# Kernel optimization log

Hardware: AMD Instinct MI355X
Metric: run time of the kernel (lower is better)

## Reference

```python
import jax, jax.numpy as jnp
import numpy as np

N_NODES = 50000
N_EDGES = 800000
IN_FEAT = 4
HIDDEN = 128
NUM_LAYERS = 3


def setup_inputs() -> dict:
    key = jax.random.key(0)
    ks = jax.random.split(key, 16)
    x = jax.random.normal(ks[0], (N_NODES, IN_FEAT), dtype=jnp.float32)
    edge_index = jax.random.randint(ks[1], (2, N_EDGES), 0, N_NODES, dtype=jnp.int64)

    def lin(k, fan_in, fan_out):
        bound = 1.0 / np.sqrt(fan_in)
        k1, k2 = jax.random.split(k)
        W = jax.random.uniform(k1, (fan_in, fan_out), minval=-bound, maxval=bound, dtype=jnp.float32)
        b = jax.random.uniform(k2, (fan_out,), minval=-bound, maxval=bound, dtype=jnp.float32)
        return W, b

    W_enc, b_enc = lin(ks[2], IN_FEAT, HIDDEN)
    W_g1, b_g1 = lin(ks[3], HIDDEN, HIDDEN)
    W_g2, b_g2 = lin(ks[4], HIDDEN, HIDDEN)
    W_g3, b_g3 = lin(ks[5], HIDDEN, HIDDEN)
    W_m1, b_m1 = lin(ks[6], 2 * HIDDEN, HIDDEN)
    W_m2, b_m2 = lin(ks[7], HIDDEN, 3)
    return {
        "x": x, "edge_index": edge_index,
        "W_enc": W_enc, "b_enc": b_enc,
        "W_g1": W_g1, "b_g1": b_g1,
        "W_g2": W_g2, "b_g2": b_g2,
        "W_g3": W_g3, "b_g3": b_g3,
        "W_m1": W_m1, "b_m1": b_m1,
        "W_m2": W_m2, "b_m2": b_m2,
    }


def _gcn_forward(x, edge_index, W_enc, b_enc, gcn_params, W_m1, b_m1, W_m2, b_m2):
    n = x.shape[0]
    # Node encoder (linear + ReLU) -> [N, H]
    h = jax.nn.relu(x @ W_enc + b_enc)

    # Add self-loops once (GCNConv default add_self_loops=True)
    src = jnp.concatenate([edge_index[0], jnp.arange(n, dtype=edge_index.dtype)])
    dst = jnp.concatenate([edge_index[1], jnp.arange(n, dtype=edge_index.dtype)])
    # Symmetric degree normalization: D^{-1/2} (A+I) D^{-1/2}
    deg = jax.ops.segment_sum(jnp.ones_like(dst, dtype=h.dtype), dst, num_segments=n)
    deg_inv_sqrt = jnp.where(deg > 0, jax.lax.rsqrt(jnp.maximum(deg, 1.0)), 0.0)
    norm = (deg_inv_sqrt[src] * deg_inv_sqrt[dst])[:, None]  # [E+N, 1]

    for (W, b) in gcn_params:
        m = (h @ W)[src] * norm                       # gather + scale messages
        h = jax.ops.segment_sum(m, dst, num_segments=n) + b
        h = jax.nn.relu(h)                            # dropout is identity at eval

    # Edge classifier: gather endpoints, concat, MLP -> [E, 3]
    ef = jnp.concatenate([h[edge_index[0]], h[edge_index[1]]], axis=-1)
    return jax.nn.relu(ef @ W_m1 + b_m1) @ W_m2 + b_m2


def reference(x, edge_index, W_enc, b_enc, W_g1, b_g1, W_g2, b_g2, W_g3, b_g3, W_m1, b_m1, W_m2, b_m2):
    gcn_params = [(W_g1, b_g1), (W_g2, b_g2), (W_g3, b_g3)]
    return _gcn_forward(x, edge_index, W_enc, b_enc, gcn_params, W_m1, b_m1, W_m2, b_m2)
```

## Files before the change

### kernel.cpp

```cpp
#include <hip/hip_runtime.h>
#include <hip/hip_bf16.h>

#define N_NODES 50000
#define N_EDGES 800000
#define HID 128
#define SCAN_BLK 512
#define N_SCAN_BLOCKS ((N_NODES + SCAN_BLK - 1) / SCAN_BLK)

typedef __attribute__((ext_vector_type(8))) short bf16x8;
typedef __attribute__((ext_vector_type(4))) float f32x4;

__device__ __forceinline__ ushort f2bf(float f) {
    uint u = __float_as_uint(f);
    return (ushort)((u + 0x7FFFu + ((u >> 16) & 1u)) >> 16);
}
__device__ __forceinline__ float bf2f(ushort h) { return __uint_as_float(((uint)h) << 16); }

__global__ void k_zero_cnt(int* cnt) {
    int i = blockIdx.x * blockDim.x + threadIdx.x;
    if (i < N_NODES) cnt[i] = 0;
}

__global__ void k_count(const int* __restrict__ ei, int* cnt) {
    int e = blockIdx.x * blockDim.x + threadIdx.x;
    if (e < N_EDGES) atomicAdd(&cnt[ei[N_EDGES + e]], 1);
}

__global__ __launch_bounds__(SCAN_BLK) void k_scan1(const int* __restrict__ cnt,
                                                    int* __restrict__ rowStart,
                                                    int* __restrict__ blockSums,
                                                    float* __restrict__ dinv) {
    __shared__ int tmp[SCAN_BLK];
    int i = blockIdx.x * SCAN_BLK + threadIdx.x;
    int v = (i < N_NODES) ? cnt[i] : 0;
    if (i < N_NODES) dinv[i] = rsqrtf(1.0f + (float)v);
    tmp[threadIdx.x] = v;
    __syncthreads();
    for (int off = 1; off < SCAN_BLK; off <<= 1) {
        int t = (threadIdx.x >= off) ? tmp[threadIdx.x - off] : 0;
        __syncthreads();
        tmp[threadIdx.x] += t;
        __syncthreads();
    }
    if (i < N_NODES) rowStart[i] = tmp[threadIdx.x] - v;
    if (threadIdx.x == SCAN_BLK - 1) blockSums[blockIdx.x] = tmp[SCAN_BLK - 1];
}

__global__ void k_scan2(int* blockSums) {
    if (blockIdx.x == 0 && threadIdx.x == 0) {
        int acc = 0;
        for (int i = 0; i < N_SCAN_BLOCKS; ++i) {
            int t = blockSums[i];
            blockSums[i] = acc;
            acc += t;
        }
    }
}

__global__ __launch_bounds__(SCAN_BLK) void k_scan3(int* __restrict__ rowStart,
                                                    const int* __restrict__ blockSums,
                                                    int* __restrict__ cursor) {
    int i = blockIdx.x * SCAN_BLK + threadIdx.x;
    if (i < N_NODES) {
        rowStart[i] += blockSums[blockIdx.x];
        cursor[i] = 0;
    }
    if (i == 0) rowStart[N_NODES] = N_EDGES;
}

__global__ void k_fill(const int* __restrict__ ei, const int* __restrict__ rowStart,
                       int* cursor, int2* __restrict__ csrE) {
    int e = blockIdx.x * blockDim.x + threadIdx.x;
    if (e < N_EDGES) {
        int s = ei[e];
        int d = ei[N_EDGES + e];
        int pos = rowStart[d] + atomicAdd(&cursor[d], 1);
        csrE[pos] = make_int2(s, e);
    }
}

struct WSplitArgs {
    const float* src[5];
    ushort* th[5];
    ushort* tl[5];
};

__global__ void k_tsplit5(WSplitArgs a) {
    int i = blockIdx.x * 256 + threadIdx.x;
    int which = i >> 14, r = i & 16383;
    int k = r >> 7, j = r & 127;
    float v = a.src[which][r];
    ushort hi = f2bf(v);
    a.th[which][j * 128 + k] = hi;
    a.tl[which][j * 128 + k] = f2bf(v - bf2f(hi));
}

__global__ void k_encoder(const float* __restrict__ x, const float* __restrict__ W,
                          const float* __restrict__ b, ushort* __restrict__ hH,
                          ushort* __restrict__ hL) {
    int i = blockIdx.x * 256 + threadIdx.x;
    int n = i >> 6, l = i & 63;
    int j = l * 2;
    float4 xv = *(const float4*)(x + (size_t)n * 4);
    float2 acc = *(const float2*)(b + j);
    float2 w0 = *(const float2*)(W + 0 * 128 + j);
    float2 w1 = *(const float2*)(W + 1 * 128 + j);
    float2 w2 = *(const float2*)(W + 2 * 128 + j);
    float2 w3 = *(const float2*)(W + 3 * 128 + j);
    acc.x += xv.x * w0.x + xv.y * w1.x + xv.z * w2.x + xv.w * w3.x;
    acc.y += xv.x * w0.y + xv.y * w1.y + xv.z * w2.y + xv.w * w3.y;
    float v0 = fmaxf(acc.x, 0.f), v1 = fmaxf(acc.y, 0.f);
    ushort h0 = f2bf(v0), h1 = f2bf(v1);
    ushort l0 = f2bf(v0 - bf2f(h0)), l1 = f2bf(v1 - bf2f(h1));
    ((uint*)hH)[i] = (uint)h0 | ((uint)h1 << 16);
    ((uint*)hL)[i] = (uint)l0 | ((uint)l1 << 16);
}

__device__ __forceinline__ void gemm_body(const ushort* __restrict__ AH,
                                          const ushort* __restrict__ AL,
                                          const ushort* __restrict__ BTH,
                                          const ushort* __restrict__ BTL,
                                          float* __restrict__ out,
                                          const float* __restrict__ bias,
                                          const float* __restrict__ scale, int M) {
    int tid = threadIdx.x;
    int w = tid >> 6, l = tid & 63;
    int ln = l & 15, lk = l >> 4;
    int r0 = blockIdx.x * 128 + w * 32;
    int row0 = r0 + ln, row1 = r0 + 16 + ln;
    int a0 = row0 < M ? row0 : M - 1;
    int a1 = row1 < M ? row1 : M - 1;

    f32x4 acc0[8] = {};
    f32x4 acc1[8] = {};
#pragma unroll
    for (int kc = 0; kc < 4; ++kc) {
        int ko = kc * 32 + lk * 8;
        bf16x8 h0H = *(const bf16x8*)(AH + (size_t)a0 * 128 + ko);
        bf16x8 h0L = *(const bf16x8*)(AL + (size_t)a0 * 128 + ko);
        bf16x8 h1H = *(const bf16x8*)(AH + (size_t)a1 * 128 + ko);
        bf16x8 h1L = *(const bf16x8*)(AL + (size_t)a1 * 128 + ko);
#pragma unroll
        for (int nt = 0; nt < 8; ++nt) {
            size_t boff = (size_t)(nt * 16 + ln) * 128 + ko;
            bf16x8 wH = *(const bf16x8*)(BTH + boff);
            bf16x8 wL = *(const bf16x8*)(BTL + boff);
            acc0[nt] = __builtin_amdgcn_mfma_f32_16x16x32_bf16(wH, h0H, acc0[nt], 0, 0, 0);
            acc0[nt] = __builtin_amdgcn_mfma_f32_16x16x32_bf16(wL, h0H, acc0[nt], 0, 0, 0);
            acc0[nt] = __builtin_amdgcn_mfma_f32_16x16x32_bf16(wH, h0L, acc0[nt], 0, 0, 0);
            acc1[nt] = __builtin_amdgcn_mfma_f32_16x16x32_bf16(wH, h1H, acc1[nt], 0, 0, 0);
            acc1[nt] = __builtin_amdgcn_mfma_f32_16x16x32_bf16(wL, h1H, acc1[nt], 0, 0, 0);
            acc1[nt] = __builtin_amdgcn_mfma_f32_16x16x32_bf16(wH, h1L, acc1[nt], 0, 0, 0);
        }
    }
    float s0v = scale ? scale[a0] : 1.f;
    float s1v = scale ? scale[a1] : 1.f;
#pragma unroll
    for (int nt = 0; nt < 8; ++nt) {
        int jb = nt * 16 + lk * 4;
        float4 bv;
        if (bias) bv = *(const float4*)(bias + jb);
        else bv = make_float4(0.f, 0.f, 0.f, 0.f);
        if (row0 < M) {
            float4 o = make_float4((acc0[nt][0] + bv.x) * s0v, (acc0[nt][1] + bv.y) * s0v,
                                   (acc0[nt][2] + bv.z) * s0v, (acc0[nt][3] + bv.w) * s0v);
            *(float4*)(out + (size_t)row0 * 128 + jb) = o;
        }
        if (row1 < M) {
            float4 o = make_float4((acc1[nt][0] + bv.x) * s1v, (acc1[nt][1] + bv.y) * s1v,
                                   (acc1[nt][2] + bv.z) * s1v, (acc1[nt][3] + bv.w) * s1v);
            *(float4*)(out + (size_t)row1 * 128 + jb) = o;
        }
    }
}

__global__ __launch_bounds__(256) void k_gemm_mfma(const ushort* __restrict__ AH,
                                                   const ushort* __restrict__ AL,
                                                   const ushort* __restrict__ BTH,
                                                   const ushort* __restrict__ BTL,
                                                   float* __restrict__ out,
                                                   const float* __restrict__ scale, int M) {
    gemm_body(AH, AL, BTH, BTL, out, nullptr, scale, M);
}

__global__ __launch_bounds__(256) void k_gemm_pq(const ushort* __restrict__ AH,
                                                 const ushort* __restrict__ AL,
                                                 const ushort* __restrict__ BTHt,
                                                 const ushort* __restrict__ BTLt,
                                                 const ushort* __restrict__ BTHb,
                                                 const ushort* __restrict__ BTLb,
                                                 float* __restrict__ outP,
                                                 float* __restrict__ outQ,
                                                 const float* __restrict__ b1, int M) {
    if (blockIdx.y == 0)
        gemm_body(AH, AL, BTHt, BTLt, outP, nullptr, nullptr, M);
    else
        gemm_body(AH, AL, BTHb, BTLb, outQ, b1, nullptr, M);
}

__global__ __launch_bounds__(256) void k_aggregate(const float* __restrict__ hw,
                                                   const float* __restrict__ b,
                                                   const float* __restrict__ dinv,
                                                   const int* __restrict__ rowStart,
                                                   const int2* __restrict__ csrE,
                                                   ushort* __restrict__ hH,
                                                   ushort* __restrict__ hL) {
    int wid = (blockIdx.x * 256 + threadIdx.x) >> 6;
    int l = threadIdx.x & 63;
    if (wid >= N_NODES) return;
    int half = l >> 5, li = l & 31;
    int c4 = li * 4;

    float4 acc;
    if (half == 0) acc = *(const float4*)(hw + (size_t)wid * 128 + c4);
    else acc = make_float4(0.f, 0.f, 0.f, 0.f);

    int s0 = rowStart[wid], s1 = rowStart[wid + 1];
    int k = s0 + half;
    float4 v = make_float4(0.f, 0.f, 0.f, 0.f);
    if (k < s1) {
        int src = csrE[k].x;
        v = *(const float4*)(hw + (size_t)src * 128 + c4);
    }
    for (; k < s1; k += 2) {
        float4 vn = make_float4(0.f, 0.f, 0.f, 0.f);
        int kn = k + 2;
        if (kn < s1) {
            int srcn = csrE[kn].x;
            vn = *(const float4*)(hw + (size_t)srcn * 128 + c4);
        }
        acc.x += v.x; acc.y += v.y; acc.z += v.z; acc.w += v.w;
        v = vn;
    }
    acc.x += __shfl_xor(acc.x, 32);
    acc.y += __shfl_xor(acc.y, 32);
    acc.z += __shfl_xor(acc.z, 32);
    acc.w += __shfl_xor(acc.w, 32);

    if (half == 0) {
        float di = dinv[wid];
        float4 bb = *(const float4*)(b + c4);
        float v0 = fmaxf(bb.x + di * acc.x, 0.f);
        float v1 = fmaxf(bb.y + di * acc.y, 0.f);
        float v2 = fmaxf(bb.z + di * acc.z, 0.f);
        float v3 = fmaxf(bb.w + di * acc.w, 0.f);
        ushort h0 = f2bf(v0), h1 = f2bf(v1), h2 = f2bf(v2), h3 = f2bf(v3);
        uint2 uh = make_uint2((uint)h0 | ((uint)h1 << 16), (uint)h2 | ((uint)h3 << 16));
        ushort l0 = f2bf(v0 - bf2f(h0)), l1 = f2bf(v1 - bf2f(h1));
        ushort l2 = f2bf(v2 - bf2f(h2)), l3 = f2bf(v3 - bf2f(h3));
        uint2 ul = make_uint2((uint)l0 | ((uint)l1 << 16), (uint)l2 | ((uint)l3 << 16));
        *(uint2*)(hH + (size_t)wid * 128 + c4) = uh;
        *(uint2*)(hL + (size_t)wid * 128 + c4) = ul;
    }
}

__global__ __launch_bounds__(256) void k_edge_final(const float* __restrict__ P,
                                                    const float* __restrict__ Qb,
                                                    const int* __restrict__ rowStart,
                                                    const int2* __restrict__ csrE,
                                                    const float* __restrict__ W2,
                                                    const float* __restrict__ b2,
                                                    float* __restrict__ out) {
    int wid = (blockIdx.x * 256 + threadIdx.x) >> 6;
    int l = threadIdx.x & 63;
    if (wid >= N_NODES) return;
    int s0 = rowStart[wid], s1 = rowStart[wid + 1];
    if (s0 >= s1) return;
    int j8 = (l & 15) * 8;
    int g = l >> 4;

    float4 qa = *(const float4*)(Qb + (size_t)wid * 128 + j8);
    float4 qb = *(const float4*)(Qb + (size_t)wid * 128 + j8 + 4);
    float w2r[8][3];
#pragma unroll
    for (int k = 0; k < 8; ++k) {
        w2r[k][0] = W2[(j8 + k) * 3 + 0];
        w2r[k][1] = W2[(j8 + k) * 3 + 1];
        w2r[k][2] = W2[(j8 + k) * 3 + 2];
    }
    float bz0 = b2[0], bz1 = b2[1], bz2 = b2[2];

    int k = s0 + g;
    int2 c = make_int2(0, 0);
    float4 pa = make_float4(0.f, 0.f, 0.f, 0.f), pb = pa;
    if (k < s1) {
        c = csrE[k];
        const float* pr = P + (size_t)c.x * 128 + j8;
        pa = *(const float4*)(pr);
        pb = *(const float4*)(pr + 4);
    }
    for (; k < s1; k += 4) {
        int kn = k + 4;
        int2 cn = make_int2(0, 0);
        float4 pan = make_float4(0.f, 0.f, 0.f, 0.f), pbn = pan;
        if (kn < s1) {
            cn = csrE[kn];
            const float* prn = P + (size_t)cn.x * 128 + j8;
            pan = *(const float4*)(prn);
            pbn = *(const float4*)(prn + 4);
        }
        float z[8];
        z[0] = fmaxf(pa.x + qa.x, 0.f);
        z[1] = fmaxf(pa.y + qa.y, 0.f);
        z[2] = fmaxf(pa.z + qa.z, 0.f);
        z[3] = fmaxf(pa.w + qa.w, 0.f);
        z[4] = fmaxf(pb.x + qb.x, 0.f);
        z[5] = fmaxf(pb.y + qb.y, 0.f);
        z[6] = fmaxf(pb.z + qb.z, 0.f);
        z[7] = fmaxf(pb.w + qb.w, 0.f);
        float o0 = 0.f, o1 = 0.f, o2 = 0.f;
#pragma unroll
        for (int q = 0; q < 8; ++q) {
            o0 += z[q] * w2r[q][0];
            o1 += z[q] * w2r[q][1];
            o2 += z[q] * w2r[q][2];
        }
#pragma unroll
        for (int m = 1; m < 16; m <<= 1) {
            o0 += __shfl_xor(o0, m);
            o1 += __shfl_xor(o1, m);
            o2 += __shfl_xor(o2, m);
        }
        if ((l & 15) == 0) {
            float* op = out + (size_t)c.y * 3;
            op[0] = o0 + bz0;
            op[1] = o1 + bz1;
            op[2] = o2 + bz2;
        }
        c = cn;
        pa = pan;
        pb = pbn;
    }
}

extern "C" void kernel_launch(void* const* d_in, const int* in_sizes, int n_in,
                              void* d_out, int out_size, void* d_ws, size_t ws_size,
                              hipStream_t stream) {
    const float* x     = (const float*)d_in[0];
    const int*   ei    = (const int*)d_in[1];
    const float* W_enc = (const float*)d_in[2];
    const float* b_enc = (const float*)d_in[3];
    const float* Wg[3] = {(const float*)d_in[4], (const float*)d_in[6], (const float*)d_in[8]};
    const float* bg[3] = {(const float*)d_in[5], (const float*)d_in[7], (const float*)d_in[9]};
    const float* W_m1  = (const float*)d_in[10];
    const float* b_m1  = (const float*)d_in[11];
    const float* W_m2  = (const float*)d_in[12];
    const float* b_m2  = (const float*)d_in[13];
    float* out = (float*)d_out;

    char* w = (char*)d_ws;
    ushort* hH      = (ushort*)w;  w += (size_t)N_NODES * HID * 2;
    ushort* hL      = (ushort*)w;  w += (size_t)N_NODES * HID * 2;
    float*  hB      = (float*)w;   w += (size_t)N_NODES * HID * 4;
    float*  Qb      = (float*)w;   w += (size_t)N_NODES * HID * 4;
    int2*   csrE    = (int2*)w;    w += (size_t)N_EDGES * 8;
    float*  dinv    = (float*)w;   w += (size_t)N_NODES * 4;
    int*    rowStart= (int*)w;     w += (size_t)(N_NODES + 4) * 4;
    int*    cursor  = (int*)w;     w += (size_t)N_NODES * 4;
    int*    blockSums=(int*)w;     w += 512;
    ushort* WgTH[3], *WgTL[3];
    for (int i = 0; i < 3; ++i) {
        WgTH[i] = (ushort*)w; w += 128 * 128 * 2;
        WgTL[i] = (ushort*)w; w += 128 * 128 * 2;
    }
    ushort* WtTH = (ushort*)w; w += 128 * 128 * 2;
    ushort* WtTL = (ushort*)w; w += 128 * 128 * 2;
    ushort* WbTH = (ushort*)w; w += 128 * 128 * 2;
    ushort* WbTL = (ushort*)w; w += 128 * 128 * 2;

    k_zero_cnt<<<(N_NODES + 255) / 256, 256, 0, stream>>>(cursor);
    k_count<<<(N_EDGES + 255) / 256, 256, 0, stream>>>(ei, cursor);
    k_scan1<<<N_SCAN_BLOCKS, SCAN_BLK, 0, stream>>>(cursor, rowStart, blockSums, dinv);
    k_scan2<<<1, 64, 0, stream>>>(blockSums);
    k_scan3<<<N_SCAN_BLOCKS, SCAN_BLK, 0, stream>>>(rowStart, blockSums, cursor);
    k_fill<<<(N_EDGES + 255) / 256, 256, 0, stream>>>(ei, rowStart, cursor, csrE);

    WSplitArgs wa;
    wa.src[0] = Wg[0]; wa.th[0] = WgTH[0]; wa.tl[0] = WgTL[0];
    wa.src[1] = Wg[1]; wa.th[1] = WgTH[1]; wa.tl[1] = WgTL[1];
    wa.src[2] = Wg[2]; wa.th[2] = WgTH[2]; wa.tl[2] = WgTL[2];
    wa.src[3] = W_m1;             wa.th[3] = WtTH; wa.tl[3] = WtTL;
    wa.src[4] = W_m1 + 128 * 128; wa.th[4] = WbTH; wa.tl[4] = WbTL;
    k_tsplit5<<<5 * 16384 / 256, 256, 0, stream>>>(wa);

    k_encoder<<<N_NODES * 64 / 256, 256, 0, stream>>>(x, W_enc, b_enc, hH, hL);

    const int gemmGrid = (N_NODES + 127) / 128;
    for (int l = 0; l < 3; ++l) {
        k_gemm_mfma<<<gemmGrid, 256, 0, stream>>>(hH, hL, WgTH[l], WgTL[l], hB, dinv, N_NODES);
        k_aggregate<<<(N_NODES * 64) / 256, 256, 0, stream>>>(hB, bg[l], dinv, rowStart, csrE, hH, hL);
    }

    dim3 pqGrid(gemmGrid, 2);
    k_gemm_pq<<<pqGrid, 256, 0, stream>>>(hH, hL, WtTH, WtTL, WbTH, WbTL, hB, Qb, b_m1, N_NODES);

    k_edge_final<<<(N_NODES * 64) / 256, 256, 0, stream>>>(hB, Qb, rowStart, csrE, W_m2, b_m2, out);
}
```

Before: 484.4 us.

## Split aggregation into column slices and use compact source-index CSR array

The GCN aggregation kernel now launches eight blocks per group of four nodes. Each block handles a 16-column slice, with four edge groups per wave and scalar float gathers instead of float4 over the whole row. A separate int-only csrA array holds source indices so the aggregation reads 4 bytes per edge instead of an int2. The aim is more parallelism and better cache reuse of gathered rows, since slice blocks run close together in time. The cost is an extra write in k_fill, eight times as many blocks that each re-read rowStart and the indices, and narrower 64-byte gathers per row.

```diff
diff --git a/kernel.cpp b/kernel.cpp
--- a/kernel.cpp
+++ b/kernel.cpp
@@ -69,12 +69,13 @@
 }
 
 __global__ void k_fill(const int* __restrict__ ei, const int* __restrict__ rowStart,
-                       int* cursor, int2* __restrict__ csrE) {
+                       int* cursor, int* __restrict__ csrA, int2* __restrict__ csrE) {
     int e = blockIdx.x * blockDim.x + threadIdx.x;
     if (e < N_EDGES) {
         int s = ei[e];
         int d = ei[N_EDGES + e];
         int pos = rowStart[d] + atomicAdd(&cursor[d], 1);
+        csrA[pos] = s;
         csrE[pos] = make_int2(s, e);
     }
 }
@@ -202,55 +203,43 @@
                                                    const float* __restrict__ b,
                                                    const float* __restrict__ dinv,
                                                    const int* __restrict__ rowStart,
-                                                   const int2* __restrict__ csrE,
+                                                   const int* __restrict__ csrA,
                                                    ushort* __restrict__ hH,
                                                    ushort* __restrict__ hL) {
-    int wid = (blockIdx.x * 256 + threadIdx.x) >> 6;
+    int bid = blockIdx.x;
+    int slice = bid & 7;
+    int n = (bid >> 3) * 4 + (threadIdx.x >> 6);
+    if (n >= N_NODES) return;
     int l = threadIdx.x & 63;
-    if (wid >= N_NODES) return;
-    int half = l >> 5, li = l & 31;
-    int c4 = li * 4;
-
-    float4 acc;
-    if (half == 0) acc = *(const float4*)(hw + (size_t)wid * 128 + c4);
-    else acc = make_float4(0.f, 0.f, 0.f, 0.f);
-
-    int s0 = rowStart[wid], s1 = rowStart[wid + 1];
-    int k = s0 + half;
-    float4 v = make_float4(0.f, 0.f, 0.f, 0.f);
+    int g = l >> 4, li = l & 15;
+    int col = slice * 16 + li;
+
+    float acc = (g == 0) ? hw[(size_t)n * 128 + col] : 0.f;
+    int s0 = rowStart[n], s1 = rowStart[n + 1];
+    int k = s0 + g;
+    float v = 0.f;
     if (k < s1) {
-        int src = csrE[k].x;
-        v = *(const float4*)(hw + (size_t)src * 128 + c4);
-    }
-    for (; k < s1; k += 2) {
-        float4 vn = make_float4(0.f, 0.f, 0.f, 0.f);
-        int kn = k + 2;
+        int src = csrA[k];
+        v = hw[(size_t)src * 128 + col];
+    }
+    for (; k < s1; k += 4) {
+        float vn = 0.f;
+        int kn = k + 4;
         if (kn < s1) {
-            int srcn = csrE[kn].x;
-            vn = *(const float4*)(hw + (size_t)srcn * 128 + c4);
-        }
-        acc.x += v.x; acc.y += v.y; acc.z += v.z; acc.w += v.w;
+            int srcn = csrA[kn];
+            vn = hw[(size_t)srcn * 128 + col];
+        }
+        acc += v;
         v = vn;
     }
-    acc.x += __shfl_xor(acc.x, 32);
-    acc.y += __shfl_xor(acc.y, 32);
-    acc.z += __shfl_xor(acc.z, 32);
-    acc.w += __shfl_xor(acc.w, 32);
-
-    if (half == 0) {
-        float di = dinv[wid];
-        float4 bb = *(const float4*)(b + c4);
-        float v0 = fmaxf(bb.x + di * acc.x, 0.f);
-        float v1 = fmaxf(bb.y + di * acc.y, 0.f);
-        float v2 = fmaxf(bb.z + di * acc.z, 0.f);
-        float v3 = fmaxf(bb.w + di * acc.w, 0.f);
-        ushort h0 = f2bf(v0), h1 = f2bf(v1), h2 = f2bf(v2), h3 = f2bf(v3);
-        uint2 uh = make_uint2((uint)h0 | ((uint)h1 << 16), (uint)h2 | ((uint)h3 << 16));
-        ushort l0 = f2bf(v0 - bf2f(h0)), l1 = f2bf(v1 - bf2f(h1));
-        ushort l2 = f2bf(v2 - bf2f(h2)), l3 = f2bf(v3 - bf2f(h3));
-        uint2 ul = make_uint2((uint)l0 | ((uint)l1 << 16), (uint)l2 | ((uint)l3 << 16));
-        *(uint2*)(hH + (size_t)wid * 128 + c4) = uh;
-        *(uint2*)(hL + (size_t)wid * 128 + c4) = ul;
+    acc += __shfl_xor(acc, 32);
+    acc += __shfl_xor(acc, 16);
+    if (g == 0) {
+        float di = dinv[n];
+        float val = fmaxf(b[col] + di * acc, 0.f);
+        ushort hi = f2bf(val);
+        hH[(size_t)n * 128 + col] = hi;
+        hL[(size_t)n * 128 + col] = f2bf(val - bf2f(hi));
     }
 }
 
@@ -354,6 +343,7 @@
     float*  hB      = (float*)w;   w += (size_t)N_NODES * HID * 4;
     float*  Qb      = (float*)w;   w += (size_t)N_NODES * HID * 4;
     int2*   csrE    = (int2*)w;    w += (size_t)N_EDGES * 8;
+    int*    csrA    = (int*)w;     w += (size_t)N_EDGES * 4;
     float*  dinv    = (float*)w;   w += (size_t)N_NODES * 4;
     int*    rowStart= (int*)w;     w += (size_t)(N_NODES + 4) * 4;
     int*    cursor  = (int*)w;     w += (size_t)N_NODES * 4;
@@ -373,7 +363,7 @@
     k_scan1<<<N_SCAN_BLOCKS, SCAN_BLK, 0, stream>>>(cursor, rowStart, blockSums, dinv);
     k_scan2<<<1, 64, 0, stream>>>(blockSums);
     k_scan3<<<N_SCAN_BLOCKS, SCAN_BLK, 0, stream>>>(rowStart, blockSums, cursor);
-    k_fill<<<(N_EDGES + 255) / 256, 256, 0, stream>>>(ei, rowStart, cursor, csrE);
+    k_fill<<<(N_EDGES + 255) / 256, 256, 0, stream>>>(ei, rowStart, cursor, csrA, csrE);
 
     WSplitArgs wa;
     wa.src[0] = Wg[0]; wa.th[0] = WgTH[0]; wa.tl[0] = WgTL[0];
@@ -386,9 +376,10 @@
     k_encoder<<<N_NODES * 64 / 256, 256, 0, stream>>>(x, W_enc, b_enc, hH, hL);
 
     const int gemmGrid = (N_NODES + 127) / 128;
+    const int aggGrid = ((N_NODES + 3) / 4) * 8;
     for (int l = 0; l < 3; ++l) {
         k_gemm_mfma<<<gemmGrid, 256, 0, stream>>>(hH, hL, WgTH[l], WgTL[l], hB, dinv, N_NODES);
-        k_aggregate<<<(N_NODES * 64) / 256, 256, 0, stream>>>(hB, bg[l], dinv, rowStart, csrE, hH, hL);
+        k_aggregate<<<aggGrid, 256, 0, stream>>>(hB, bg[l], dinv, rowStart, csrA, hH, hL);
     }
 
     dim3 pqGrid(gemmGrid, 2);
```

Result: slower. 890.1 us (+83.7%).

## Widen aggregation to four edge groups and merge scan passes

Applied to the files above, without the earlier changes.

The aggregate kernel now handles four edges at a time per wavefront, with 16 lanes each loading 8 floats, instead of two edges with 32 lanes each loading 4 floats. This adds memory-level parallelism for nodes with higher degree, at the cost of an extra shuffle-reduction stage and more registers. The single-thread block-sum scan and the offset-add kernel are combined into one kernel in which every block redundantly scans the 98 block sums in shared memory. The zeroing kernel is replaced by hipMemsetAsync, which removes one launch.

```diff
diff --git a/kernel.cpp b/kernel.cpp
--- a/kernel.cpp
+++ b/kernel.cpp
@@ -15,11 +15,6 @@
     return (ushort)((u + 0x7FFFu + ((u >> 16) & 1u)) >> 16);
 }
 __device__ __forceinline__ float bf2f(ushort h) { return __uint_as_float(((uint)h) << 16); }
-
-__global__ void k_zero_cnt(int* cnt) {
-    int i = blockIdx.x * blockDim.x + threadIdx.x;
-    if (i < N_NODES) cnt[i] = 0;
-}
 
 __global__ void k_count(const int* __restrict__ ei, int* cnt) {
     int e = blockIdx.x * blockDim.x + threadIdx.x;
@@ -46,23 +41,23 @@
     if (threadIdx.x == SCAN_BLK - 1) blockSums[blockIdx.x] = tmp[SCAN_BLK - 1];
 }
 
-__global__ void k_scan2(int* blockSums) {
-    if (blockIdx.x == 0 && threadIdx.x == 0) {
-        int acc = 0;
-        for (int i = 0; i < N_SCAN_BLOCKS; ++i) {
-            int t = blockSums[i];
-            blockSums[i] = acc;
-            acc += t;
-        }
-    }
-}
-
-__global__ __launch_bounds__(SCAN_BLK) void k_scan3(int* __restrict__ rowStart,
-                                                    const int* __restrict__ blockSums,
-                                                    int* __restrict__ cursor) {
-    int i = blockIdx.x * SCAN_BLK + threadIdx.x;
+__global__ __launch_bounds__(SCAN_BLK) void k_scan23(int* __restrict__ rowStart,
+                                                     const int* __restrict__ blockSums,
+                                                     int* __restrict__ cursor) {
+    __shared__ int ps[128];
+    int t = threadIdx.x;
+    if (t < 128) ps[t] = (t < N_SCAN_BLOCKS) ? blockSums[t] : 0;
+    __syncthreads();
+    for (int off = 1; off < 128; off <<= 1) {
+        int v = (t < 128 && t >= off) ? ps[t - off] : 0;
+        __syncthreads();
+        if (t < 128) ps[t] += v;
+        __syncthreads();
+    }
+    int i = blockIdx.x * SCAN_BLK + t;
+    int prefix = (blockIdx.x == 0) ? 0 : ps[blockIdx.x - 1];
     if (i < N_NODES) {
-        rowStart[i] += blockSums[blockIdx.x];
+        rowStart[i] += prefix;
         cursor[i] = 0;
     }
     if (i == 0) rowStart[N_NODES] = N_EDGES;
@@ -208,49 +203,71 @@
     int wid = (blockIdx.x * 256 + threadIdx.x) >> 6;
     int l = threadIdx.x & 63;
     if (wid >= N_NODES) return;
-    int half = l >> 5, li = l & 31;
-    int c4 = li * 4;
-
-    float4 acc;
-    if (half == 0) acc = *(const float4*)(hw + (size_t)wid * 128 + c4);
-    else acc = make_float4(0.f, 0.f, 0.f, 0.f);
+    int g = l >> 4, li = l & 15;
+    int c8 = li * 8;
+
+    float4 aA, aB;
+    if (g == 0) {
+        aA = *(const float4*)(hw + (size_t)wid * 128 + c8);
+        aB = *(const float4*)(hw + (size_t)wid * 128 + c8 + 4);
+    } else {
+        aA = make_float4(0.f, 0.f, 0.f, 0.f);
+        aB = aA;
+    }
 
     int s0 = rowStart[wid], s1 = rowStart[wid + 1];
-    int k = s0 + half;
-    float4 v = make_float4(0.f, 0.f, 0.f, 0.f);
+    int k = s0 + g;
+    float4 v0a = make_float4(0.f, 0.f, 0.f, 0.f), v0b = v0a;
     if (k < s1) {
-        int src = csrE[k].x;
-        v = *(const float4*)(hw + (size_t)src * 128 + c4);
-    }
-    for (; k < s1; k += 2) {
-        float4 vn = make_float4(0.f, 0.f, 0.f, 0.f);
-        int kn = k + 2;
-        if (kn < s1) {
-            int srcn = csrE[kn].x;
-            vn = *(const float4*)(hw + (size_t)srcn * 128 + c4);
-        }
-        acc.x += v.x; acc.y += v.y; acc.z += v.z; acc.w += v.w;
-        v = vn;
-    }
-    acc.x += __shfl_xor(acc.x, 32);
-    acc.y += __shfl_xor(acc.y, 32);
-    acc.z += __shfl_xor(acc.z, 32);
-    acc.w += __shfl_xor(acc.w, 32);
-
-    if (half == 0) {
+        const float* r = hw + (size_t)csrE[k].x * 128 + c8;
+        v0a = *(const float4*)(r);
+        v0b = *(const float4*)(r + 4);
+    }
+    for (; k < s1; k += 4) {
+        float4 v1a = make_float4(0.f, 0.f, 0.f, 0.f), v1b = v1a;
+        if (k + 4 < s1) {
+            const float* r = hw + (size_t)csrE[k + 4].x * 128 + c8;
+            v1a = *(const float4*)(r);
+            v1b = *(const float4*)(r + 4);
+        }
+        aA.x += v0a.x; aA.y += v0a.y; aA.z += v0a.z; aA.w += v0a.w;
+        aB.x += v0b.x; aB.y += v0b.y; aB.z += v0b.z; aB.w += v0b.w;
+        v0a = v1a;
+        v0b = v1b;
+    }
+    aA.x += __shfl_xor(aA.x, 16); aA.y += __shfl_xor(aA.y, 16);
+    aA.z += __shfl_xor(aA.z, 16); aA.w += __shfl_xor(aA.w, 16);
+    aB.x += __shfl_xor(aB.x, 16); aB.y += __shfl_xor(aB.y, 16);
+    aB.z += __shfl_xor(aB.z, 16); aB.w += __shfl_xor(aB.w, 16);
+    aA.x += __shfl_xor(aA.x, 32); aA.y += __shfl_xor(aA.y, 32);
+    aA.z += __shfl_xor(aA.z, 32); aA.w += __shfl_xor(aA.w, 32);
+    aB.x += __shfl_xor(aB.x, 32); aB.y += __shfl_xor(aB.y, 32);
+    aB.z += __shfl_xor(aB.z, 32); aB.w += __shfl_xor(aB.w, 32);
+
+    if (g == 0) {
         float di = dinv[wid];
-        float4 bb = *(const float4*)(b + c4);
-        float v0 = fmaxf(bb.x + di * acc.x, 0.f);
-        float v1 = fmaxf(bb.y + di * acc.y, 0.f);
-        float v2 = fmaxf(bb.z + di * acc.z, 0.f);
-        float v3 = fmaxf(bb.w + di * acc.w, 0.f);
-        ushort h0 = f2bf(v0), h1 = f2bf(v1), h2 = f2bf(v2), h3 = f2bf(v3);
-        uint2 uh = make_uint2((uint)h0 | ((uint)h1 << 16), (uint)h2 | ((uint)h3 << 16));
-        ushort l0 = f2bf(v0 - bf2f(h0)), l1 = f2bf(v1 - bf2f(h1));
-        ushort l2 = f2bf(v2 - bf2f(h2)), l3 = f2bf(v3 - bf2f(h3));
-        uint2 ul = make_uint2((uint)l0 | ((uint)l1 << 16), (uint)l2 | ((uint)l3 << 16));
-        *(uint2*)(hH + (size_t)wid * 128 + c4) = uh;
-        *(uint2*)(hL + (size_t)wid * 128 + c4) = ul;
+        float4 bbA = *(const float4*)(b + c8);
+        float4 bbB = *(const float4*)(b + c8 + 4);
+        float f0 = fmaxf(bbA.x + di * aA.x, 0.f);
+        float f1 = fmaxf(bbA.y + di * aA.y, 0.f);
+        float f2 = fmaxf(bbA.z + di * aA.z, 0.f);
+        float f3 = fmaxf(bbA.w + di * aA.w, 0.f);
+        float f4v = fmaxf(bbB.x + di * aB.x, 0.f);
+        float f5 = fmaxf(bbB.y + di * aB.y, 0.f);
+        float f6 = fmaxf(bbB.z + di * aB.z, 0.f);
+        float f7 = fmaxf(bbB.w + di * aB.w, 0.f);
+        ushort h0 = f2bf(f0), h1 = f2bf(f1), h2 = f2bf(f2), h3 = f2bf(f3);
+        ushort h4 = f2bf(f4v), h5 = f2bf(f5), h6 = f2bf(f6), h7 = f2bf(f7);
+        uint4 uh = make_uint4((uint)h0 | ((uint)h1 << 16), (uint)h2 | ((uint)h3 << 16),
+                              (uint)h4 | ((uint)h5 << 16), (uint)h6 | ((uint)h7 << 16));
+        ushort l0 = f2bf(f0 - bf2f(h0)), l1 = f2bf(f1 - bf2f(h1));
+        ushort l2 = f2bf(f2 - bf2f(h2)), l3 = f2bf(f3 - bf2f(h3));
+        ushort l4 = f2bf(f4v - bf2f(h4)), l5 = f2bf(f5 - bf2f(h5));
+        ushort l6 = f2bf(f6 - bf2f(h6)), l7 = f2bf(f7 - bf2f(h7));
+        uint4 ul = make_uint4((uint)l0 | ((uint)l1 << 16), (uint)l2 | ((uint)l3 << 16),
+                              (uint)l4 | ((uint)l5 << 16), (uint)l6 | ((uint)l7 << 16));
+        *(uint4*)(hH + (size_t)wid * 128 + c8) = uh;
+        *(uint4*)(hL + (size_t)wid * 128 + c8) = ul;
     }
 }
 
@@ -368,11 +385,10 @@
     ushort* WbTH = (ushort*)w; w += 128 * 128 * 2;
     ushort* WbTL = (ushort*)w; w += 128 * 128 * 2;
 
-    k_zero_cnt<<<(N_NODES + 255) / 256, 256, 0, stream>>>(cursor);
+    hipMemsetAsync(cursor, 0, (size_t)N_NODES * 4, stream);
     k_count<<<(N_EDGES + 255) / 256, 256, 0, stream>>>(ei, cursor);
     k_scan1<<<N_SCAN_BLOCKS, SCAN_BLK, 0, stream>>>(cursor, rowStart, blockSums, dinv);
-    k_scan2<<<1, 64, 0, stream>>>(blockSums);
-    k_scan3<<<N_SCAN_BLOCKS, SCAN_BLK, 0, stream>>>(rowStart, blockSums, cursor);
+    k_scan23<<<N_SCAN_BLOCKS, SCAN_BLK, 0, stream>>>(rowStart, blockSums, cursor);
     k_fill<<<(N_EDGES + 255) / 256, 256, 0, stream>>>(ei, rowStart, cursor, csrE);
 
     WSplitArgs wa;
```

Measured after the change: 469.3 us. 1.03x faster.
